# Performance work log

Measured on AMD Instinct MI355X. Metric: run time of the kernel, lower is better.

Reference implementation:

```python
import jax, jax.numpy as jnp
import numpy as np
from jax import lax

C = 256

def conv1x1(x, w, b):
    # x: [B,C,H,W], w: [O,C], b: [O]
    return jnp.einsum('bchw,oc->bohw', x, w) + b[None, :, None, None]

def conv3x3_s2(x, w, b):
    # x: [B,C,H,W], w: [O,C,3,3] -> stride 2, pad 1
    y = lax.conv_general_dilated(x, w, window_strides=(2, 2),
                                 padding=((1, 1), (1, 1)),
                                 dimension_numbers=('NCHW', 'OIHW', 'NCHW'))
    return y + b[None, :, None, None]

def to_qv(x):
    # [B,C,H,W] -> permute(0,2,3,1) -> view [B,H,W,1,C]
    return jnp.transpose(x, (0, 2, 3, 1))[:, :, :, None, :]

def to_k(x):
    # [B,C,H,W] -> permute(0,2,3,1) -> view [B,H,W,C,1]
    return jnp.transpose(x, (0, 2, 3, 1))[:, :, :, :, None]

def upsample2x_nearest(x):
    return jnp.repeat(jnp.repeat(x, 2, axis=2), 2, axis=3)


def setup_inputs() -> dict:
    key = jax.random.key(0)
    ks = jax.random.split(key, 20)
    x1 = jax.random.normal(ks[0], (2, C, 128, 128), dtype=jnp.float32)
    x2 = jax.random.normal(ks[1], (2, C, 64, 64), dtype=jnp.float32)
    s = 0.05
    d = {'x1': x1, 'x2': x2}
    names = ['q1', 'q2', 'ks1', 'ks2', 'kup', 'v1', 'v2']
    for i, n in enumerate(names):
        d[n + '_w'] = jax.random.normal(ks[2 + 2 * i], (C, C), dtype=jnp.float32) * s
        d[n + '_b'] = jax.random.normal(ks[3 + 2 * i], (C,), dtype=jnp.float32) * s
    d['kdown_w'] = jax.random.normal(ks[16], (C, C, 3, 3), dtype=jnp.float32) * s
    d['kdown_b'] = jax.random.normal(ks[17], (C,), dtype=jnp.float32) * s
    return d


def reference(x1, x2, q1_w, q1_b, q2_w, q2_b, ks1_w, ks1_b, ks2_w, ks2_b,
              kup_w, kup_b, v1_w, v1_b, v2_w, v2_b, kdown_w, kdown_b):
    q1 = to_qv(conv1x1(x1, q1_w, q1_b))            # [B,128,128,1,C]
    q2 = to_qv(conv1x1(x2, q2_w, q2_b))            # [B,64,64,1,C]
    k_up = to_k(upsample2x_nearest(conv1x1(x2, kup_w, kup_b)))  # [B,128,128,C,1]
    k_self_1 = to_k(conv1x1(x1, ks1_w, ks1_b))     # [B,128,128,C,1]
    k_self_2 = to_k(conv1x1(x2, ks2_w, ks2_b))     # [B,64,64,C,1]
    k_down = to_k(conv3x3_s2(x1, kdown_w, kdown_b))  # [B,64,64,C,1]
    v1 = to_qv(conv1x1(x1, v1_w, v1_b))            # [B,128,128,1,C]
    v2 = to_qv(conv1x1(x2, v2_w, v2_b))            # [B,64,64,1,C]
    return (q1, q2, k_up, k_self_1, k_self_2, k_down, v1, v2)
```

## Files before the change

### kernel.cpp

```cpp
#include <hip/hip_runtime.h>
#include <hip/hip_bf16.h>
#include <stdint.h>


typedef __attribute__((ext_vector_type(8))) __bf16 bf16x8;
typedef __attribute__((ext_vector_type(4))) float f32x4;
typedef __attribute__((ext_vector_type(8))) unsigned short u16x8;

typedef const __attribute__((address_space(1))) uint32_t* gptr_t;
typedef __attribute__((address_space(3))) uint32_t* lptr_t;

__device__ __forceinline__ void cp16(void* lds, const void* g) {
  gptr_t gp = reinterpret_cast<gptr_t>(reinterpret_cast<uintptr_t>(g));
  lptr_t lp = reinterpret_cast<lptr_t>(
      static_cast<uint32_t>(reinterpret_cast<uintptr_t>(lds)));
  __builtin_amdgcn_global_load_lds(gp, lp, 16, 0, 0);
}

struct WArgs {
  const float* w1[7];
  const float* kdw;
};

__global__ void prep_transpose(WArgs a, const float* __restrict__ x1,
                               const float* __restrict__ x2,
                               uint16_t* __restrict__ wf,
                               uint16_t* __restrict__ x1p,
                               uint16_t* __restrict__ x2b) {
  __shared__ float tile[64][65];
  const int bx = blockIdx.x;
  const int tid = threadIdx.x;
  if (bx < 512) {
    const int idx = bx * 256 + tid;
    const int mat = idx >> 13;
    const int g = idx & 8191;
    const int jg = g >> 9;
    const int kc = (g >> 6) & 7;
    const int lane = g & 63;
    const int o = jg * 16 + (lane & 15);
    const int k0 = kc * 32 + (lane >> 4) * 8;
    float f[8];
    if (mat < 7) {
      const float* w = a.w1[mat];
      const float4 v0 = *(const float4*)(w + o * 256 + k0);
      const float4 v1 = *(const float4*)(w + o * 256 + k0 + 4);
      f[0] = v0.x; f[1] = v0.y; f[2] = v0.z; f[3] = v0.w;
      f[4] = v1.x; f[5] = v1.y; f[6] = v1.z; f[7] = v1.w;
    } else {
      const int tap = mat - 7;
#pragma unroll
      for (int e = 0; e < 8; e++)
        f[e] = a.kdw[(long)o * 2304 + (long)(k0 + e) * 9 + tap];
    }
    u16x8 u;
#pragma unroll
    for (int e = 0; e < 8; e++) {
      __hip_bfloat16 hb = __float2bfloat16(f[e]);
      u[e] = *reinterpret_cast<uint16_t*>(&hb);
    }
    *(u16x8*)(wf + (long)idx * 8) = u;
    return;
  }
  if (bx < 641) {
    const int c = (bx - 512) * 256 + tid;
    const int b = (c >= 16512) ? 1 : 0;
    const int cc = c - b * 16512;
    int h, w, g8;
    if (cc < 4160) {
      h = 0; w = cc >> 5; g8 = cc & 31;
    } else if (cc < 8320) {
      const int s = cc - 4160; h = 129; w = s >> 5; g8 = s & 31;
    } else if (cc < 12416) {
      const int s = cc - 8320; h = 1 + (s >> 5); w = 0; g8 = s & 31;
    } else {
      const int s = cc - 12416; h = 1 + (s >> 5); w = 129; g8 = s & 31;
    }
    u16x8 z = {};
    *(u16x8*)(x1p + (((long)(b * 130 + h)) * 130 + w) * 256 + g8 * 8) = z;
    return;
  }
  const int t = bx - 641;
  const float* src;
  uint16_t* dst;
  int H, W, pad, b, h, bxx, by;
  if (t < 2048) {
    src = x1; dst = x1p; H = 128; W = 128; pad = 1;
    bxx = t & 1; by = (t >> 1) & 3;
    const int z = t >> 3; b = z >> 7; h = z & 127;
  } else {
    const int t2 = t - 2048;
    src = x2; dst = x2b; H = 64; W = 64; pad = 0;
    bxx = 0; by = t2 & 3;
    const int z = t2 >> 2;
    b = z >> 6; h = z & 63;
  }
  const int wt = bxx * 64;
  const int ct = by * 64;
  const long cs = (long)H * W;
  const float* s = src + ((long)(b * 256 + ct) * H + h) * W + wt;
  const int rw = tid >> 4;
  const int rf = tid & 15;
#pragma unroll
  for (int p = 0; p < 4; p++) {
    const int cl = p * 16 + rw;
    const float4 v = *(const float4*)(s + (long)cl * cs + rf * 4);
    tile[cl][rf * 4 + 0] = v.x;
    tile[cl][rf * 4 + 1] = v.y;
    tile[cl][rf * 4 + 2] = v.z;
    tile[cl][rf * 4 + 3] = v.w;
  }
  __syncthreads();
  const int wl0 = tid >> 3;
  const int cg = tid & 7;
  const int Wp = W + 2 * pad;
  const long rowb = ((long)(b * (H + 2 * pad) + h + pad)) * Wp + pad + wt;
#pragma unroll
  for (int p = 0; p < 2; p++) {
    const int wl = p * 32 + wl0;
    u16x8 u;
#pragma unroll
    for (int k = 0; k < 8; k++) {
      __hip_bfloat16 hb = __float2bfloat16(tile[cg * 8 + k][wl]);
      u[k] = *reinterpret_cast<uint16_t*>(&hb);
    }
    *(u16x8*)(dst + (rowb + wl) * 256 + ct + cg * 8) = u;
  }
}

struct Job {
  const uint16_t* A;
  const uint16_t* Wf;
  const float* bias;
  float* out;
  int start;
  int mode;
};
struct JobArgs {
  Job j[8];
};

__global__ __launch_bounds__(256, 2) void fused_gemm(JobArgs args) {
  int jid = 0;
#pragma unroll
  for (int t = 1; t < 8; t++)
    if ((int)blockIdx.x >= args.j[t].start) jid = t;
  const Job jb = args.j[jid];
  const int bid = blockIdx.x - jb.start;
  const int mode = jb.mode;

  __shared__ __align__(16) uint16_t lA[32768];

  const int tid = threadIdx.x;
  const int lane = tid & 63;
  const int wave = tid >> 6;
  const int wr = wave & 1;
  const int wc = wave >> 1;
  const int q = lane >> 4;
  const int l15 = lane & 15;
  const int ksel = ((lane & 3) ^ ((lane >> 3) & 3)) * 8;
  const int qsw = (q ^ ((l15 >> 1) & 3)) * 8;

  if (mode == 3) {
    const int mtile = bid >> 1;
    const int ntile = bid & 1;
    const int row = mtile * 64 + wave * 16 + (lane >> 2);
    const long p =
        ((long)((row >> 12) * 130 + 2 * ((row >> 6) & 63))) * 130 + 2 * (row & 63);
    const uint16_t* rowA = jb.A + p * 256 + ksel;

    f32x4 acc[2][4] = {};
    for (int tap = 0; tap < 9; tap++) {
      const int kh = tap / 3;
      const int kw = tap - kh * 3;
      const long aoff = (long)(kh * 130 + kw) * 256;
      const uint16_t* wfp = jb.Wf + (long)tap * 65536;
      if (tap) __syncthreads();
#pragma unroll
      for (int kap = 0; kap < 8; kap++)
        cp16(lA + (kap * 256 + wave * 64) * 8, rowA + aoff + kap * 32);
      __syncthreads();
#pragma unroll
      for (int kc = 0; kc < 8; kc++) {
        bf16x8 av[2];
#pragma unroll
        for (int i = 0; i < 2; i++)
          av[i] = *(const bf16x8*)(lA + (kc * 64 + wr * 32 + i * 16 + l15) * 32 + qsw);
#pragma unroll
        for (int j = 0; j < 4; j++) {
          const bf16x8 bv = *(const bf16x8*)(
              wfp + ((long)((ntile * 8 + wc * 4 + j) * 8 + kc) * 64 + lane) * 8);
#pragma unroll
          for (int i = 0; i < 2; i++)
            acc[i][j] = __builtin_amdgcn_mfma_f32_16x16x32_bf16(bv, av[i],
                                                                acc[i][j], 0, 0, 0);
        }
      }
    }
    const int nb2 = ntile * 128 + wc * 64 + q * 4;
    const int mb2 = mtile * 64 + wr * 32 + l15;
#pragma unroll
    for (int j = 0; j < 4; j++) {
      const int n = nb2 + j * 16;
      const f32x4 bq = *(const f32x4*)(jb.bias + n);
#pragma unroll
      for (int i = 0; i < 2; i++) {
        const int m = mb2 + i * 16;
        *(f32x4*)(jb.out + (long)m * 256 + n) = acc[i][j] + bq;
      }
    }
    return;
  }

  const int mtile = bid;
  const uint16_t* rowA[2];
  {
    const int rbase = wave * 16 + (lane >> 2);
#pragma unroll
    for (int rh = 0; rh < 2; rh++) {
      const int m = mtile * 128 + rh * 64 + rbase;
      long p;
      if (mode == 0) {
        p = ((long)((m >> 14) * 130 + ((m >> 7) & 127) + 1)) * 130 + (m & 127) + 1;
      } else {
        p = m;
      }
      rowA[rh] = jb.A + p * 256 + ksel;
    }
  }

#pragma unroll
  for (int kap = 0; kap < 16; kap++)
    cp16(lA + (kap * 256 + wave * 64) * 8, rowA[kap & 1] + (kap >> 1) * 32);
  __syncthreads();

  f32x4 acc[4][8] = {};
#pragma unroll
  for (int kc = 0; kc < 8; kc++) {
    bf16x8 av[4];
#pragma unroll
    for (int i = 0; i < 4; i++)
      av[i] = *(const bf16x8*)(lA + (kc * 128 + wr * 64 + i * 16 + l15) * 32 + qsw);
#pragma unroll
    for (int j = 0; j < 8; j++) {
      const bf16x8 bv =
          *(const bf16x8*)(jb.Wf + ((long)((wc * 8 + j) * 8 + kc) * 64 + lane) * 8);
#pragma unroll
      for (int i = 0; i < 4; i++)
        acc[i][j] = __builtin_amdgcn_mfma_f32_16x16x32_bf16(bv, av[i],
                                                            acc[i][j], 0, 0, 0);
    }
  }

  const int nb2 = wc * 128 + q * 4;
  const int mb2 = mtile * 128 + wr * 64 + l15;
  if (mode == 2) {
#pragma unroll
    for (int j = 0; j < 8; j++) {
      const int n = nb2 + j * 16;
      const f32x4 bq = *(const f32x4*)(jb.bias + n);
#pragma unroll
      for (int i = 0; i < 4; i++) {
        const int m = mb2 + i * 16;
        const int b = m >> 12;
        const int h2 = (m >> 6) & 63;
        const int w2 = m & 63;
        const f32x4 v = acc[i][j] + bq;
        float* o = jb.out + ((long)(b * 128 + 2 * h2) * 128 + 2 * w2) * 256 + n;
        *(f32x4*)(o) = v;
        *(f32x4*)(o + 256) = v;
        *(f32x4*)(o + 32768) = v;
        *(f32x4*)(o + 32768 + 256) = v;
      }
    }
  } else {
#pragma unroll
    for (int j = 0; j < 8; j++) {
      const int n = nb2 + j * 16;
      const f32x4 bq = *(const f32x4*)(jb.bias + n);
#pragma unroll
      for (int i = 0; i < 4; i++) {
        const int m = mb2 + i * 16;
        *(f32x4*)(jb.out + (long)m * 256 + n) = acc[i][j] + bq;
      }
    }
  }
}

extern "C" void kernel_launch(void* const* d_in, const int* in_sizes, int n_in,
                              void* d_out, int out_size, void* d_ws,
                              size_t ws_size, hipStream_t stream) {
  (void)in_sizes; (void)n_in; (void)out_size; (void)ws_size;
  const float* x1 = (const float*)d_in[0];
  const float* x2 = (const float*)d_in[1];
  float* out = (float*)d_out;

  uint16_t* x1p = (uint16_t*)d_ws;
  uint16_t* x2b = x1p + 8652800;
  uint16_t* wf = x2b + 2097152;

  WArgs wa;
  wa.w1[0] = (const float*)d_in[2];
  wa.w1[1] = (const float*)d_in[4];
  wa.w1[2] = (const float*)d_in[6];
  wa.w1[3] = (const float*)d_in[8];
  wa.w1[4] = (const float*)d_in[10];
  wa.w1[5] = (const float*)d_in[12];
  wa.w1[6] = (const float*)d_in[14];
  wa.kdw = (const float*)d_in[16];
  prep_transpose<<<3201, 256, 0, stream>>>(wa, x1, x2, wf, x1p, x2b);

  JobArgs ja;
  ja.j[0] = {x1p, wf + 7 * 65536, (const float*)d_in[17], out + 29360128L, 0,    3};
  ja.j[1] = {x1p, wf + 0 * 65536, (const float*)d_in[3],  out + 0L,        256,  0};
  ja.j[2] = {x1p, wf + 2 * 65536, (const float*)d_in[7],  out + 18874368L, 512,  0};
  ja.j[3] = {x1p, wf + 5 * 65536, (const float*)d_in[13], out + 31457280L, 768,  0};
  ja.j[4] = {x2b, wf + 4 * 65536, (const float*)d_in[11], out + 10485760L, 1024, 2};
  ja.j[5] = {x2b, wf + 1 * 65536, (const float*)d_in[5],  out + 8388608L,  1088, 1};
  ja.j[6] = {x2b, wf + 3 * 65536, (const float*)d_in[9],  out + 27262976L, 1152, 1};
  ja.j[7] = {x2b, wf + 6 * 65536, (const float*)d_in[15], out + 39845888L, 1216, 1};
  fused_gemm<<<1280, 256, 0, stream>>>(ja);
}
```

Before: 299.4 us.

## Reuse loaded activation tile across all weight matrices sharing the same input

Instead of launching one block per (job, m-tile), each block loads its 128-row activation tile into LDS once and loops over the 3 (x1) or 4 (x2) 1x1-conv weight matrices that consume that input. Grid shrinks from 1280 to 576 blocks. The aim is to avoid reloading the same A tile from global memory for every projection. In exchange there are fewer blocks to spread across CUs and each block does serial work, which may reduce parallelism and latency hiding.

```diff
diff --git a/kernel.cpp b/kernel.cpp
--- a/kernel.cpp
+++ b/kernel.cpp
@@ -127,26 +127,18 @@
   }
 }
 
-struct Job {
-  const uint16_t* A;
-  const uint16_t* Wf;
-  const float* bias;
-  float* out;
-  int start;
-  int mode;
+struct GArgs {
+  const uint16_t* x1p;
+  const uint16_t* x2b;
+  const uint16_t* wf;
+  const float* b_q1; const float* b_q2; const float* b_ks1; const float* b_ks2;
+  const float* b_kup; const float* b_v1; const float* b_v2; const float* b_kd;
+  float* o_q1; float* o_q2; float* o_ks1; float* o_ks2;
+  float* o_kup; float* o_v1; float* o_v2; float* o_kd;
 };
-struct JobArgs {
-  Job j[8];
-};
-
-__global__ __launch_bounds__(256, 2) void fused_gemm(JobArgs args) {
-  int jid = 0;
-#pragma unroll
-  for (int t = 1; t < 8; t++)
-    if ((int)blockIdx.x >= args.j[t].start) jid = t;
-  const Job jb = args.j[jid];
-  const int bid = blockIdx.x - jb.start;
-  const int mode = jb.mode;
+
+__global__ __launch_bounds__(256, 2) void fused_gemm(GArgs a) {
+  const int bid = blockIdx.x;
 
   __shared__ __align__(16) uint16_t lA[32768];
 
@@ -160,20 +152,20 @@
   const int ksel = ((lane & 3) ^ ((lane >> 3) & 3)) * 8;
   const int qsw = (q ^ ((l15 >> 1) & 3)) * 8;
 
-  if (mode == 3) {
+  if (bid < 256) {
     const int mtile = bid >> 1;
     const int ntile = bid & 1;
     const int row = mtile * 64 + wave * 16 + (lane >> 2);
     const long p =
         ((long)((row >> 12) * 130 + 2 * ((row >> 6) & 63))) * 130 + 2 * (row & 63);
-    const uint16_t* rowA = jb.A + p * 256 + ksel;
+    const uint16_t* rowA = a.x1p + p * 256 + ksel;
 
     f32x4 acc[2][4] = {};
     for (int tap = 0; tap < 9; tap++) {
       const int kh = tap / 3;
       const int kw = tap - kh * 3;
       const long aoff = (long)(kh * 130 + kw) * 256;
-      const uint16_t* wfp = jb.Wf + (long)tap * 65536;
+      const uint16_t* wfp = a.wf + (long)(7 + tap) * 65536;
       if (tap) __syncthreads();
 #pragma unroll
       for (int kap = 0; kap < 8; kap++)
@@ -201,86 +193,108 @@
 #pragma unroll
     for (int j = 0; j < 4; j++) {
       const int n = nb2 + j * 16;
-      const f32x4 bq = *(const f32x4*)(jb.bias + n);
+      const f32x4 bq = *(const f32x4*)(a.b_kd + n);
 #pragma unroll
       for (int i = 0; i < 2; i++) {
         const int m = mb2 + i * 16;
-        *(f32x4*)(jb.out + (long)m * 256 + n) = acc[i][j] + bq;
+        *(f32x4*)(a.o_kd + (long)m * 256 + n) = acc[i][j] + bq;
       }
     }
     return;
   }
 
-  const int mtile = bid;
-  const uint16_t* rowA[2];
+  const int x1grp = (bid < 512) ? 1 : 0;
+  const int mtile = x1grp ? (bid - 256) : (bid - 512);
+  const uint16_t* A = x1grp ? a.x1p : a.x2b;
+  const int njobs = x1grp ? 3 : 4;
+
   {
     const int rbase = wave * 16 + (lane >> 2);
+    const uint16_t* rowA[2];
 #pragma unroll
     for (int rh = 0; rh < 2; rh++) {
       const int m = mtile * 128 + rh * 64 + rbase;
       long p;
-      if (mode == 0) {
+      if (x1grp) {
         p = ((long)((m >> 14) * 130 + ((m >> 7) & 127) + 1)) * 130 + (m & 127) + 1;
       } else {
         p = m;
       }
-      rowA[rh] = jb.A + p * 256 + ksel;
-    }
-  }
-
-#pragma unroll
-  for (int kap = 0; kap < 16; kap++)
-    cp16(lA + (kap * 256 + wave * 64) * 8, rowA[kap & 1] + (kap >> 1) * 32);
+      rowA[rh] = A + p * 256 + ksel;
+    }
+#pragma unroll
+    for (int kap = 0; kap < 16; kap++)
+      cp16(lA + (kap * 256 + wave * 64) * 8, rowA[kap & 1] + (kap >> 1) * 32);
+  }
   __syncthreads();
 
-  f32x4 acc[4][8] = {};
-#pragma unroll
-  for (int kc = 0; kc < 8; kc++) {
-    bf16x8 av[4];
-#pragma unroll
-    for (int i = 0; i < 4; i++)
-      av[i] = *(const bf16x8*)(lA + (kc * 128 + wr * 64 + i * 16 + l15) * 32 + qsw);
-#pragma unroll
-    for (int j = 0; j < 8; j++) {
-      const bf16x8 bv =
-          *(const bf16x8*)(jb.Wf + ((long)((wc * 8 + j) * 8 + kc) * 64 + lane) * 8);
+#pragma unroll 1
+  for (int jj = 0; jj < njobs; jj++) {
+    int mat;
+    const float* bias;
+    float* outp;
+    int ups = 0;
+    if (x1grp) {
+      if (jj == 0)      { mat = 0; bias = a.b_q1;  outp = a.o_q1;  }
+      else if (jj == 1) { mat = 2; bias = a.b_ks1; outp = a.o_ks1; }
+      else              { mat = 5; bias = a.b_v1;  outp = a.o_v1;  }
+    } else {
+      if (jj == 0)      { mat = 1; bias = a.b_q2;  outp = a.o_q2;  }
+      else if (jj == 1) { mat = 3; bias = a.b_ks2; outp = a.o_ks2; }
+      else if (jj == 2) { mat = 6; bias = a.b_v2;  outp = a.o_v2;  }
+      else              { mat = 4; bias = a.b_kup; outp = a.o_kup; ups = 1; }
+    }
+    const uint16_t* Wf = a.wf + (long)mat * 65536;
+
+    f32x4 acc[4][8] = {};
+#pragma unroll
+    for (int kc = 0; kc < 8; kc++) {
+      bf16x8 av[4];
 #pragma unroll
       for (int i = 0; i < 4; i++)
-        acc[i][j] = __builtin_amdgcn_mfma_f32_16x16x32_bf16(bv, av[i],
-                                                            acc[i][j], 0, 0, 0);
-    }
-  }
-
-  const int nb2 = wc * 128 + q * 4;
-  const int mb2 = mtile * 128 + wr * 64 + l15;
-  if (mode == 2) {
-#pragma unroll
-    for (int j = 0; j < 8; j++) {
-      const int n = nb2 + j * 16;
-      const f32x4 bq = *(const f32x4*)(jb.bias + n);
-#pragma unroll
-      for (int i = 0; i < 4; i++) {
-        const int m = mb2 + i * 16;
-        const int b = m >> 12;
-        const int h2 = (m >> 6) & 63;
-        const int w2 = m & 63;
-        const f32x4 v = acc[i][j] + bq;
-        float* o = jb.out + ((long)(b * 128 + 2 * h2) * 128 + 2 * w2) * 256 + n;
-        *(f32x4*)(o) = v;
-        *(f32x4*)(o + 256) = v;
-        *(f32x4*)(o + 32768) = v;
-        *(f32x4*)(o + 32768 + 256) = v;
-      }
-    }
-  } else {
-#pragma unroll
-    for (int j = 0; j < 8; j++) {
-      const int n = nb2 + j * 16;
-      const f32x4 bq = *(const f32x4*)(jb.bias + n);
-#pragma unroll
-      for (int i = 0; i < 4; i++) {
-        const int m = mb2 + i * 16;
-        *(f32x4*)(jb.out + (long)m * 256 + n) = acc[i][j] + bq;
+        av[i] = *(const bf16x8*)(lA + (kc * 128 + wr * 64 + i * 16 + l15) * 32 + qsw);
+#pragma unroll
+      for (int j = 0; j < 8; j++) {
+        const bf16x8 bv =
+            *(const bf16x8*)(Wf + ((long)((wc * 8 + j) * 8 + kc) * 64 + lane) * 8);
+#pragma unroll
+        for (int i = 0; i < 4; i++)
+          acc[i][j] = __builtin_amdgcn_mfma_f32_16x16x32_bf16(bv, av[i],
+                                                              acc[i][j], 0, 0, 0);
+      }
+    }
+
+    const int nb2 = wc * 128 + q * 4;
+    const int mb2 = mtile * 128 + wr * 64 + l15;
+    if (ups) {
+#pragma unroll
+      for (int j = 0; j < 8; j++) {
+        const int n = nb2 + j * 16;
+        const f32x4 bq = *(const f32x4*)(bias + n);
+#pragma unroll
+        for (int i = 0; i < 4; i++) {
+          const int m = mb2 + i * 16;
+          const int b = m >> 12;
+          const int h2 = (m >> 6) & 63;
+          const int w2 = m & 63;
+          const f32x4 v = acc[i][j] + bq;
+          float* o = outp + ((long)(b * 128 + 2 * h2) * 128 + 2 * w2) * 256 + n;
+          *(f32x4*)(o) = v;
+          *(f32x4*)(o + 256) = v;
+          *(f32x4*)(o + 32768) = v;
+          *(f32x4*)(o + 32768 + 256) = v;
+        }
+      }
+    } else {
+#pragma unroll
+      for (int j = 0; j < 8; j++) {
+        const int n = nb2 + j * 16;
+        const f32x4 bq = *(const f32x4*)(bias + n);
+#pragma unroll
+        for (int i = 0; i < 4; i++) {
+          const int m = mb2 + i * 16;
+          *(f32x4*)(outp + (long)m * 256 + n) = acc[i][j] + bq;
+        }
       }
     }
   }
@@ -309,14 +323,23 @@
   wa.kdw = (const float*)d_in[16];
   prep_transpose<<<3201, 256, 0, stream>>>(wa, x1, x2, wf, x1p, x2b);
 
-  JobArgs ja;
-  ja.j[0] = {x1p, wf + 7 * 65536, (const float*)d_in[17], out + 29360128L, 0,    3};
-  ja.j[1] = {x1p, wf + 0 * 65536, (const float*)d_in[3],  out + 0L,        256,  0};
-  ja.j[2] = {x1p, wf + 2 * 65536, (const float*)d_in[7],  out + 18874368L, 512,  0};
-  ja.j[3] = {x1p, wf + 5 * 65536, (const float*)d_in[13], out + 31457280L, 768,  0};
-  ja.j[4] = {x2b, wf + 4 * 65536, (const float*)d_in[11], out + 10485760L, 1024, 2};
-  ja.j[5] = {x2b, wf + 1 * 65536, (const float*)d_in[5],  out + 8388608L,  1088, 1};
-  ja.j[6] = {x2b, wf + 3 * 65536, (const float*)d_in[9],  out + 27262976L, 1152, 1};
-  ja.j[7] = {x2b, wf + 6 * 65536, (const float*)d_in[15], out + 39845888L, 1216, 1};
-  fused_gemm<<<1280, 256, 0, stream>>>(ja);
+  GArgs ga;
+  ga.x1p = x1p; ga.x2b = x2b; ga.wf = wf;
+  ga.b_q1  = (const float*)d_in[3];
+  ga.b_q2  = (const float*)d_in[5];
+  ga.b_ks1 = (const float*)d_in[7];
+  ga.b_ks2 = (const float*)d_in[9];
+  ga.b_kup = (const float*)d_in[11];
+  ga.b_v1  = (const float*)d_in[13];
+  ga.b_v2  = (const float*)d_in[15];
+  ga.b_kd  = (const float*)d_in[17];
+  ga.o_q1  = out + 0L;
+  ga.o_q2  = out + 8388608L;
+  ga.o_kup = out + 10485760L;
+  ga.o_ks1 = out + 18874368L;
+  ga.o_ks2 = out + 27262976L;
+  ga.o_kd  = out + 29360128L;
+  ga.o_v1  = out + 31457280L;
+  ga.o_v2  = out + 39845888L;
+  fused_gemm<<<576, 256, 0, stream>>>(ga);
 }
```

Measured after the change: 366.6 us. 1.22x slower.
